# Optimization experiments

Measured on AMD Instinct MI355X. Metric: run time of the kernel, lower is better.

## Reference

```python
import jax, jax.numpy as jnp
import numpy as np

HID, NH, HD = 2048, 16, 128


def setup_inputs() -> dict:
    key = jax.random.key(0)
    ks = jax.random.split(key, 9)
    B, S = 2, 2048
    std = 0.02
    return {
        "hidden_states": jax.random.normal(ks[0], (B, S, HID), dtype=jnp.float32),
        "Wq": jax.random.normal(ks[1], (HID, HID), dtype=jnp.float32) * std,
        "bq": jnp.zeros((HID,), dtype=jnp.float32),
        "Wk": jax.random.normal(ks[2], (HID, HID), dtype=jnp.float32) * std,
        "bk": jnp.zeros((HID,), dtype=jnp.float32),
        "Wv": jax.random.normal(ks[3], (HID, HID), dtype=jnp.float32) * std,
        "bv": jnp.zeros((HID,), dtype=jnp.float32),
        "Wo": jax.random.normal(ks[4], (HID, HID), dtype=jnp.float32) * std,
        "bo": jnp.zeros((HID,), dtype=jnp.float32),
    }


def reference(hidden_states, Wq, bq, Wk, bk, Wv, bv, Wo, bo):
    B, S, _ = hidden_states.shape
    # torch Linear: x @ W.T + b
    def proj(W, b):
        y = hidden_states @ W.T + b
        return y.reshape(B, S, NH, HD).transpose(0, 2, 1, 3)  # (B, NH, S, HD)

    q = proj(Wq, bq)
    k = proj(Wk, bk)
    v = proj(Wv, bv)

    scale = jnp.float32(np.sqrt(HD))
    scores = jnp.einsum("bhqd,bhkd->bhqk", q, k) / scale  # (B, NH, S, S)
    causal = jnp.triu(jnp.ones((S, S), dtype=bool), k=1)
    scores = jnp.where(causal, jnp.float32(-jnp.inf), scores)
    weights = jax.nn.softmax(scores, axis=-1)
    out = jnp.einsum("bhqk,bhkd->bhqd", weights, v)  # (B, NH, S, HD)
    out = out.transpose(0, 2, 1, 3).reshape(B, S, HID)
    return out @ Wo.T + bo
```

## Files before the change

### kernel.cpp

```cpp
#include <hip/hip_runtime.h>
#include <hip/hip_bf16.h>

#define BATCH 2
#define SEQ   2048
#define HID_  2048
#define NH_   16
#define HD_   128

typedef __bf16 bf16x8 __attribute__((ext_vector_type(8)));
typedef float  f32x4  __attribute__((ext_vector_type(4)));

__device__ __forceinline__ unsigned short f32_to_bf16(float f) {
    unsigned int u = __builtin_bit_cast(unsigned int, f);
    unsigned int r = (u + 0x7fffu + ((u >> 16) & 1u)) >> 16;
    return (unsigned short)r;
}

__device__ __forceinline__ void gld_lds16(void* lds, const void* g) {
    __builtin_amdgcn_global_load_lds(
        (const __attribute__((address_space(1))) unsigned int*)g,
        (__attribute__((address_space(3))) unsigned int*)lds, 16, 0, 0);
}

__global__ void cvt_f32_bf16(const float* __restrict__ in,
                             unsigned short* __restrict__ out, int n4) {
    int i = blockIdx.x * blockDim.x + threadIdx.x;
    if (i >= n4) return;
    float4 a = reinterpret_cast<const float4*>(in)[i];
    ushort4 o;
    o.x = f32_to_bf16(a.x);
    o.y = f32_to_bf16(a.y);
    o.z = f32_to_bf16(a.z);
    o.w = f32_to_bf16(a.w);
    reinterpret_cast<ushort4*>(out)[i] = o;
}

enum { OUT_BF16 = 0, OUT_VT = 1, OUT_F32 = 2 };

template <int MODE>
__global__ __launch_bounds__(256)
void gemm_bt(const unsigned short* __restrict__ A,
             const unsigned short* __restrict__ B,
             const float* __restrict__ bias,
             void* __restrict__ Cout,
             int M, int N, int K) {
    const int tid  = threadIdx.x;
    const int lane = tid & 63;
    const int wid  = tid >> 6;
    const int wr   = wid >> 1;
    const int wc   = wid & 1;
    const int l16  = lane & 15;
    const int l4   = lane >> 4;

    const int row0 = blockIdx.y * 128;
    const int col0 = blockIdx.x * 128;

    __shared__ unsigned short As[128 * 32];
    __shared__ unsigned short Bs[128 * 32];

    f32x4 acc[4][4] = {};

    const int srow = tid >> 2;
    const int scol = (tid & 3) * 8;
    const unsigned short* Ag = A + (size_t)(row0 + srow) * K + scol;
    const unsigned short* Bg = B + (size_t)(col0 + srow) * K + scol;
    unsigned short* AsW = As + wid * 512;
    unsigned short* BsW = Bs + wid * 512;

    const unsigned short* AsR = As + (size_t)(wr * 64 + l16) * 32 + l4 * 8;
    const unsigned short* BsR = Bs + (size_t)(wc * 64 + l16) * 32 + l4 * 8;

    for (int k0 = 0; k0 < K; k0 += 32) {
        __syncthreads();
        gld_lds16(AsW,        Ag + k0);
        gld_lds16(AsW + 2048, Ag + (size_t)64 * K + k0);
        gld_lds16(BsW,        Bg + k0);
        gld_lds16(BsW + 2048, Bg + (size_t)64 * K + k0);
        __syncthreads();

        bf16x8 af[4], bfr[4];
#pragma unroll
        for (int i = 0; i < 4; ++i)
            af[i] = *reinterpret_cast<const bf16x8*>(AsR + i * 16 * 32);
#pragma unroll
        for (int j = 0; j < 4; ++j)
            bfr[j] = *reinterpret_cast<const bf16x8*>(BsR + j * 16 * 32);
#pragma unroll
        for (int i = 0; i < 4; ++i)
#pragma unroll
            for (int j = 0; j < 4; ++j)
                acc[i][j] = __builtin_amdgcn_mfma_f32_16x16x32_bf16(
                    af[i], bfr[j], acc[i][j], 0, 0, 0);
    }

    const int wrow0 = row0 + wr * 64;
    const int wcol0 = col0 + wc * 64;
#pragma unroll
    for (int j = 0; j < 4; ++j) {
        const int col = wcol0 + j * 16 + l16;
        const float bv = bias[col];
#pragma unroll
        for (int i = 0; i < 4; ++i) {
#pragma unroll
            for (int r = 0; r < 4; ++r) {
                const int row = wrow0 + i * 16 + l4 * 4 + r;
                const float v = acc[i][j][r] + bv;
                if (MODE == OUT_BF16) {
                    ((unsigned short*)Cout)[(size_t)row * N + col] = f32_to_bf16(v);
                } else if (MODE == OUT_F32) {
                    ((float*)Cout)[(size_t)row * N + col] = v;
                } else {
                    const int b = row >> 11, s = row & (SEQ - 1);
                    const int h = col >> 7,  d = col & (HD_ - 1);
                    ((unsigned short*)Cout)[((size_t)((b * NH_ + h) * HD_ + d)) * SEQ + s] =
                        f32_to_bf16(v);
                }
            }
        }
    }
}

__global__ __launch_bounds__(256, 2)
void attn_fwd(const unsigned short* __restrict__ Qm,
              const unsigned short* __restrict__ Km,
              const unsigned short* __restrict__ Vt,
              unsigned short* __restrict__ Om) {
    const int tid  = threadIdx.x;
    const int lane = tid & 63;
    const int wq   = tid >> 6;
    const int l16  = lane & 15;
    const int l4   = lane >> 4;

    const int bh = blockIdx.x;
    const int qt = (int)gridDim.y - 1 - (int)blockIdx.y;
    const int b  = bh >> 4;
    const int h  = bh & (NH_ - 1);

    const int qbase  = qt * 64 + wq * 16;
    const int ntiles = qt + 1;

    __shared__ unsigned short Ks[2][64 * 128];
    __shared__ unsigned short Vs[2][128 * 64];
    __shared__ unsigned short plds[4][16][68];

    const unsigned short* Kbh = Km + ((size_t)b * SEQ) * HID_ + h * HD_;
    const unsigned short* Vbh = Vt + (size_t)bh * HD_ * SEQ;

    auto stage = [&](int buf, int t) {
        const int kv0 = t * 64;
        {
            const int rl = lane >> 4;
            const int ck = lane & 15;
#pragma unroll
            for (int j = 0; j < 4; ++j) {
                const int r  = wq * 16 + 4 * j + rl;
                const int lc = ck ^ (r & 7);
                gld_lds16(&Ks[buf][(wq * 16 + 4 * j) * 128],
                          Kbh + (size_t)(kv0 + r) * HID_ + lc * 8);
            }
        }
        {
            const int rl = lane >> 3;
            const int ck = lane & 7;
#pragma unroll
            for (int j = 0; j < 4; ++j) {
                const int r  = wq * 32 + 8 * j + rl;
                const int lc = ck ^ (r & 7);
                gld_lds16(&Vs[buf][(wq * 32 + 8 * j) * 64],
                          Vbh + (size_t)r * SEQ + kv0 + lc * 8);
            }
        }
    };

    stage(0, 0);
    const unsigned short* Qbase =
        Qm + ((size_t)(b * SEQ + qbase + l16)) * HID_ + h * HD_ + l4 * 8;
    bf16x8 qf[4];
#pragma unroll
    for (int kb = 0; kb < 4; ++kb)
        qf[kb] = *reinterpret_cast<const bf16x8*>(Qbase + kb * 32);

    float mrow[4], lrow[4];
#pragma unroll
    for (int r = 0; r < 4; ++r) { mrow[r] = -__builtin_inff(); lrow[r] = 0.f; }
    f32x4 acc[8] = {};

    const float scale = 0.08838834764831845f;

    int buf = 0;
    for (int t = 0; t < ntiles; ++t) {
        __syncthreads();
        if (t + 1 < ntiles) stage(buf ^ 1, t + 1);

        const unsigned short* Kb0 = &Ks[buf][0];
        const unsigned short* Vb0 = &Vs[buf][0];
        const int kv0 = t * 64;
        const int sw  = l16 & 7;

        f32x4 sc[4];
#pragma unroll
        for (int ct = 0; ct < 4; ++ct) {
            f32x4 c = {};
#pragma unroll
            for (int kb = 0; kb < 4; ++kb) {
                bf16x8 kf = *reinterpret_cast<const bf16x8*>(
                    Kb0 + (ct * 16 + l16) * 128 + ((kb * 4 + l4) ^ sw) * 8);
                c = __builtin_amdgcn_mfma_f32_16x16x32_bf16(qf[kb], kf, c, 0, 0, 0);
            }
            sc[ct] = c;
        }

        if (t == ntiles - 1) {
#pragma unroll
            for (int ct = 0; ct < 4; ++ct) {
                const int col = kv0 + ct * 16 + l16;
#pragma unroll
                for (int r = 0; r < 4; ++r) {
                    float v = sc[ct][r] * scale;
                    const int qrow = qbase + l4 * 4 + r;
                    if (col > qrow) v = -__builtin_inff();
                    sc[ct][r] = v;
                }
            }
        } else {
#pragma unroll
            for (int ct = 0; ct < 4; ++ct)
#pragma unroll
                for (int r = 0; r < 4; ++r)
                    sc[ct][r] *= scale;
        }

        float tmax[4];
#pragma unroll
        for (int r = 0; r < 4; ++r) {
            float v = fmaxf(fmaxf(sc[0][r], sc[1][r]), fmaxf(sc[2][r], sc[3][r]));
#pragma unroll
            for (int off = 8; off >= 1; off >>= 1)
                v = fmaxf(v, __shfl_xor(v, off, 64));
            tmax[r] = v;
        }

        float alpha[4], rs[4];
#pragma unroll
        for (int r = 0; r < 4; ++r) {
            const float mn = fmaxf(mrow[r], tmax[r]);
            alpha[r] = __expf(mrow[r] - mn);
            mrow[r] = mn;
            rs[r] = 0.f;
        }

#pragma unroll
        for (int ct = 0; ct < 4; ++ct) {
#pragma unroll
            for (int r = 0; r < 4; ++r) {
                const float p = __expf(sc[ct][r] - mrow[r]);
                rs[r] += p;
                plds[wq][l4 * 4 + r][ct * 16 + l16] = f32_to_bf16(p);
            }
        }

#pragma unroll
        for (int r = 0; r < 4; ++r) {
#pragma unroll
            for (int off = 8; off >= 1; off >>= 1)
                rs[r] += __shfl_xor(rs[r], off, 64);
            lrow[r] = lrow[r] * alpha[r] + rs[r];
        }

#pragma unroll
        for (int dt = 0; dt < 8; ++dt)
#pragma unroll
            for (int r = 0; r < 4; ++r)
                acc[dt][r] *= alpha[r];

        asm volatile("s_waitcnt lgkmcnt(0)" ::: "memory");
        bf16x8 pf[2];
#pragma unroll
        for (int ks = 0; ks < 2; ++ks)
            pf[ks] = *reinterpret_cast<const bf16x8*>(&plds[wq][l16][ks * 32 + l4 * 8]);
#pragma unroll
        for (int dt = 0; dt < 8; ++dt) {
#pragma unroll
            for (int ks = 0; ks < 2; ++ks) {
                bf16x8 vf = *reinterpret_cast<const bf16x8*>(
                    Vb0 + (dt * 16 + l16) * 64 + ((ks * 4 + l4) ^ sw) * 8);
                acc[dt] = __builtin_amdgcn_mfma_f32_16x16x32_bf16(pf[ks], vf, acc[dt], 0, 0, 0);
            }
        }

        buf ^= 1;
    }

    unsigned short* Ob = Om + ((size_t)(b * SEQ + qbase)) * HID_ + h * HD_;
#pragma unroll
    for (int dt = 0; dt < 8; ++dt) {
#pragma unroll
        for (int r = 0; r < 4; ++r) {
            const int qrow = l4 * 4 + r;
            const float v = acc[dt][r] / lrow[r];
            Ob[(size_t)qrow * HID_ + dt * 16 + l16] = f32_to_bf16(v);
        }
    }
}

extern "C" void kernel_launch(void* const* d_in, const int* in_sizes, int n_in,
                              void* d_out, int out_size, void* d_ws, size_t ws_size,
                              hipStream_t stream) {
    const float* X  = (const float*)d_in[0];
    const float* Wq = (const float*)d_in[1];
    const float* bq = (const float*)d_in[2];
    const float* Wk = (const float*)d_in[3];
    const float* bk = (const float*)d_in[4];
    const float* Wv = (const float*)d_in[5];
    const float* bv = (const float*)d_in[6];
    const float* Wo = (const float*)d_in[7];
    const float* bo = (const float*)d_in[8];
    float* out = (float*)d_out;

    const size_t MK = (size_t)BATCH * SEQ * HID_;
    const size_t WK = (size_t)HID_ * HID_;

    unsigned short* ws  = (unsigned short*)d_ws;
    unsigned short* Xb  = ws;
    unsigned short* Wqb = Xb  + MK;
    unsigned short* Wkb = Wqb + WK;
    unsigned short* Wvb = Wkb + WK;
    unsigned short* Wob = Wvb + WK;
    unsigned short* Qb  = Wob + WK;
    unsigned short* Kb  = Qb  + MK;
    unsigned short* Vtb = Kb  + MK;
    unsigned short* AOb = Vtb + MK;

    auto cvt = [&](const float* src, unsigned short* dst, size_t n) {
        int n4 = (int)(n / 4);
        cvt_f32_bf16<<<(n4 + 255) / 256, 256, 0, stream>>>(src, dst, n4);
    };
    cvt(X,  Xb,  MK);
    cvt(Wq, Wqb, WK);
    cvt(Wk, Wkb, WK);
    cvt(Wv, Wvb, WK);
    cvt(Wo, Wob, WK);

    const int M = BATCH * SEQ;
    dim3 g(HID_ / 128, M / 128);

    gemm_bt<OUT_BF16><<<g, 256, 0, stream>>>(Xb, Wqb, bq, Qb,  M, HID_, HID_);
    gemm_bt<OUT_BF16><<<g, 256, 0, stream>>>(Xb, Wkb, bk, Kb,  M, HID_, HID_);
    gemm_bt<OUT_VT>  <<<g, 256, 0, stream>>>(Xb, Wvb, bv, Vtb, M, HID_, HID_);

    attn_fwd<<<dim3(BATCH * NH_, SEQ / 64), 256, 0, stream>>>(Qb, Kb, Vtb, AOb);

    gemm_bt<OUT_F32><<<g, 256, 0, stream>>>(AOb, Wob, bo, out, M, HID_, HID_);
}
```

Baseline: 455.4 us.

## Double-buffer GEMM loads, swizzle LDS, fuse QKV GEMMs, lazy softmax rescale

The GEMM main loop now double-buffers LDS tiles so the next K-slice loads while MFMAs run, and applies an XOR swizzle to LDS columns to cut bank conflicts. The Q, K and V projections become one launch over a 3x wider grid, with the output segment chosen per block. This relies on Wq, Wk and Wv sitting contiguously in the bf16 buffer. Flash attention skips rescaling the running max and accumulators unless the new tile max exceeds the old one by more than 8, trading exp/multiply work for a bounded risk of overflow in the accumulators.

Result: faster. 433.2 us (-4.9%).

```diff
diff --git a/kernel.cpp b/kernel.cpp
--- a/kernel.cpp
+++ b/kernel.cpp
@@ -35,64 +35,109 @@
     reinterpret_cast<ushort4*>(out)[i] = o;
 }
 
-enum { OUT_BF16 = 0, OUT_VT = 1, OUT_F32 = 2 };
-
-template <int MODE>
+#define GEMM_MAIN_LOOP                                                       \
+    const int K = HID_;                                                      \
+    const int tid  = threadIdx.x;                                            \
+    const int lane = tid & 63;                                               \
+    const int wid  = tid >> 6;                                               \
+    const int wr   = wid >> 1;                                               \
+    const int wc   = wid & 1;                                                \
+    const int l16  = lane & 15;                                              \
+    const int l4   = lane >> 4;                                              \
+    const int ckey = l16 & 3;                                                \
+    const int row0 = blockIdx.y * 128;                                       \
+    const int col0 = blockIdx.x * 128;                                       \
+    __shared__ unsigned short As[2][128 * 32];                               \
+    __shared__ unsigned short Bs[2][128 * 32];                               \
+    f32x4 acc[4][4] = {};                                                    \
+    const int srow = tid >> 2;                                               \
+    const int scol = ((tid & 3) ^ (srow & 3)) * 8;     \
+    const unsigned short* Ag = A + (size_t)(row0 + srow) * K + scol;         \
+    const unsigned short* Bg = B + (size_t)(col0 + srow) * K + scol;         \
+    auto stage = [&](int bb, int k0) {                                       \
+        gld_lds16(&As[bb][wid * 512],        Ag + k0);                       \
+        gld_lds16(&As[bb][2048 + wid * 512], Ag + (size_t)64 * K + k0);      \
+        gld_lds16(&Bs[bb][wid * 512],        Bg + k0);                       \
+        gld_lds16(&Bs[bb][2048 + wid * 512], Bg + (size_t)64 * K + k0);      \
+    };                                                                       \
+    stage(0, 0);                                                             \
+    int buf = 0;                                                             \
+    for (int k0 = 0; k0 < K; k0 += 32) {                                     \
+        const bool more = (k0 + 32) < K;                                     \
+        if (more) {                                                          \
+            stage(buf ^ 1, k0 + 32);                                         \
+            asm volatile("s_waitcnt vmcnt(4)" ::: "memory");                 \
+        } else {                                                             \
+            asm volatile("s_waitcnt vmcnt(0)" ::: "memory");                 \
+        }                                                                    \
+        __builtin_amdgcn_s_barrier();                                        \
+        const unsigned short* Ab = &As[buf][0];                              \
+        const unsigned short* Bb = &Bs[buf][0];                              \
+        bf16x8 af[4], bfr[4];                                                \
+        _Pragma("unroll")                                                    \
+        for (int i = 0; i < 4; ++i)                                          \
+            af[i] = *reinterpret_cast<const bf16x8*>(                        \
+                Ab + (wr * 64 + i * 16 + l16) * 32 + ((l4 ^ ckey) * 8));     \
+        _Pragma("unroll")                                                    \
+        for (int j = 0; j < 4; ++j)                                          \
+            bfr[j] = *reinterpret_cast<const bf16x8*>(                       \
+                Bb + (wc * 64 + j * 16 + l16) * 32 + ((l4 ^ ckey) * 8));     \
+        _Pragma("unroll")                                                    \
+        for (int i = 0; i < 4; ++i)                                          \
+            _Pragma("unroll")                                                \
+            for (int j = 0; j < 4; ++j)                                      \
+                acc[i][j] = __builtin_amdgcn_mfma_f32_16x16x32_bf16(         \
+                    af[i], bfr[j], acc[i][j], 0, 0, 0);                      \
+        asm volatile("s_waitcnt lgkmcnt(0)" ::: "memory");                   \
+        __builtin_amdgcn_s_barrier();                                        \
+        buf ^= 1;                                                            \
+    }
+
 __global__ __launch_bounds__(256)
-void gemm_bt(const unsigned short* __restrict__ A,
-             const unsigned short* __restrict__ B,
-             const float* __restrict__ bias,
-             void* __restrict__ Cout,
-             int M, int N, int K) {
-    const int tid  = threadIdx.x;
-    const int lane = tid & 63;
-    const int wid  = tid >> 6;
-    const int wr   = wid >> 1;
-    const int wc   = wid & 1;
-    const int l16  = lane & 15;
-    const int l4   = lane >> 4;
-
-    const int row0 = blockIdx.y * 128;
-    const int col0 = blockIdx.x * 128;
-
-    __shared__ unsigned short As[128 * 32];
-    __shared__ unsigned short Bs[128 * 32];
-
-    f32x4 acc[4][4] = {};
-
-    const int srow = tid >> 2;
-    const int scol = (tid & 3) * 8;
-    const unsigned short* Ag = A + (size_t)(row0 + srow) * K + scol;
-    const unsigned short* Bg = B + (size_t)(col0 + srow) * K + scol;
-    unsigned short* AsW = As + wid * 512;
-    unsigned short* BsW = Bs + wid * 512;
-
-    const unsigned short* AsR = As + (size_t)(wr * 64 + l16) * 32 + l4 * 8;
-    const unsigned short* BsR = Bs + (size_t)(wc * 64 + l16) * 32 + l4 * 8;
-
-    for (int k0 = 0; k0 < K; k0 += 32) {
-        __syncthreads();
-        gld_lds16(AsW,        Ag + k0);
-        gld_lds16(AsW + 2048, Ag + (size_t)64 * K + k0);
-        gld_lds16(BsW,        Bg + k0);
-        gld_lds16(BsW + 2048, Bg + (size_t)64 * K + k0);
-        __syncthreads();
-
-        bf16x8 af[4], bfr[4];
-#pragma unroll
-        for (int i = 0; i < 4; ++i)
-            af[i] = *reinterpret_cast<const bf16x8*>(AsR + i * 16 * 32);
-#pragma unroll
-        for (int j = 0; j < 4; ++j)
-            bfr[j] = *reinterpret_cast<const bf16x8*>(BsR + j * 16 * 32);
-#pragma unroll
-        for (int i = 0; i < 4; ++i)
-#pragma unroll
-            for (int j = 0; j < 4; ++j)
-                acc[i][j] = __builtin_amdgcn_mfma_f32_16x16x32_bf16(
-                    af[i], bfr[j], acc[i][j], 0, 0, 0);
-    }
-
+void gemm_qkv(const unsigned short* __restrict__ A,
+              const unsigned short* __restrict__ B,
+              const float* __restrict__ bq,
+              const float* __restrict__ bk,
+              const float* __restrict__ bv,
+              unsigned short* __restrict__ Qo,
+              unsigned short* __restrict__ Ko,
+              unsigned short* __restrict__ Vto) {
+    GEMM_MAIN_LOOP
+    const int seg = col0 >> 11;
+    const float* bias = (seg == 0) ? bq : (seg == 1) ? bk : bv;
+    const int wrow0 = row0 + wr * 64;
+    const int wcol0 = (col0 & (HID_ - 1)) + wc * 64;
+#pragma unroll
+    for (int j = 0; j < 4; ++j) {
+        const int col = wcol0 + j * 16 + l16;
+        const float bvv = bias[col];
+#pragma unroll
+        for (int i = 0; i < 4; ++i) {
+#pragma unroll
+            for (int r = 0; r < 4; ++r) {
+                const int row = wrow0 + i * 16 + l4 * 4 + r;
+                const float v = acc[i][j][r] + bvv;
+                if (seg == 0) {
+                    Qo[(size_t)row * HID_ + col] = f32_to_bf16(v);
+                } else if (seg == 1) {
+                    Ko[(size_t)row * HID_ + col] = f32_to_bf16(v);
+                } else {
+                    const int b = row >> 11, s = row & (SEQ - 1);
+                    const int h = col >> 7,  d = col & (HD_ - 1);
+                    Vto[((size_t)((b * NH_ + h) * HD_ + d)) * SEQ + s] =
+                        f32_to_bf16(v);
+                }
+            }
+        }
+    }
+}
+
+__global__ __launch_bounds__(256)
+void gemm_out(const unsigned short* __restrict__ A,
+              const unsigned short* __restrict__ B,
+              const float* __restrict__ bias,
+              float* __restrict__ Cout) {
+    GEMM_MAIN_LOOP
     const int wrow0 = row0 + wr * 64;
     const int wcol0 = col0 + wc * 64;
 #pragma unroll
@@ -104,17 +149,7 @@
 #pragma unroll
             for (int r = 0; r < 4; ++r) {
                 const int row = wrow0 + i * 16 + l4 * 4 + r;
-                const float v = acc[i][j][r] + bv;
-                if (MODE == OUT_BF16) {
-                    ((unsigned short*)Cout)[(size_t)row * N + col] = f32_to_bf16(v);
-                } else if (MODE == OUT_F32) {
-                    ((float*)Cout)[(size_t)row * N + col] = v;
-                } else {
-                    const int b = row >> 11, s = row & (SEQ - 1);
-                    const int h = col >> 7,  d = col & (HD_ - 1);
-                    ((unsigned short*)Cout)[((size_t)((b * NH_ + h) * HD_ + d)) * SEQ + s] =
-                        f32_to_bf16(v);
-                }
+                Cout[(size_t)row * HID_ + col] = acc[i][j][r] + bv;
             }
         }
     }
@@ -240,15 +275,25 @@
             tmax[r] = v;
         }
 
-        float alpha[4], rs[4];
-#pragma unroll
-        for (int r = 0; r < 4; ++r) {
-            const float mn = fmaxf(mrow[r], tmax[r]);
-            alpha[r] = __expf(mrow[r] - mn);
-            mrow[r] = mn;
-            rs[r] = 0.f;
-        }
-
+        bool need = false;
+#pragma unroll
+        for (int r = 0; r < 4; ++r) need = need || (tmax[r] > mrow[r] + 8.f);
+        if (__any(need)) {
+#pragma unroll
+            for (int r = 0; r < 4; ++r) {
+                const float mn = fmaxf(mrow[r], tmax[r]);
+                const float al = __expf(mrow[r] - mn);
+                mrow[r] = mn;
+                lrow[r] *= al;
+#pragma unroll
+                for (int dt = 0; dt < 8; ++dt)
+                    acc[dt][r] *= al;
+            }
+        }
+
+        float rs[4];
+#pragma unroll
+        for (int r = 0; r < 4; ++r) rs[r] = 0.f;
 #pragma unroll
         for (int ct = 0; ct < 4; ++ct) {
 #pragma unroll
@@ -264,14 +309,8 @@
 #pragma unroll
             for (int off = 8; off >= 1; off >>= 1)
                 rs[r] += __shfl_xor(rs[r], off, 64);
-            lrow[r] = lrow[r] * alpha[r] + rs[r];
-        }
-
-#pragma unroll
-        for (int dt = 0; dt < 8; ++dt)
-#pragma unroll
-            for (int r = 0; r < 4; ++r)
-                acc[dt][r] *= alpha[r];
+            lrow[r] += rs[r];
+        }
 
         asm volatile("s_waitcnt lgkmcnt(0)" ::: "memory");
         bf16x8 pf[2];
@@ -341,14 +380,11 @@
     cvt(Wv, Wvb, WK);
     cvt(Wo, Wob, WK);
 
-    const int M = BATCH * SEQ;
-    dim3 g(HID_ / 128, M / 128);
-
-    gemm_bt<OUT_BF16><<<g, 256, 0, stream>>>(Xb, Wqb, bq, Qb,  M, HID_, HID_);
-    gemm_bt<OUT_BF16><<<g, 256, 0, stream>>>(Xb, Wkb, bk, Kb,  M, HID_, HID_);
-    gemm_bt<OUT_VT>  <<<g, 256, 0, stream>>>(Xb, Wvb, bv, Vtb, M, HID_, HID_);
+    gemm_qkv<<<dim3(3 * HID_ / 128, BATCH * SEQ / 128), 256, 0, stream>>>(
+        Xb, Wqb, bq, bk, bv, Qb, Kb, Vtb);
 
     attn_fwd<<<dim3(BATCH * NH_, SEQ / 64), 256, 0, stream>>>(Qb, Kb, Vtb, AOb);
 
-    gemm_bt<OUT_F32><<<g, 256, 0, stream>>>(AOb, Wob, bo, out, M, HID_, HID_);
-}
+    gemm_out<<<dim3(HID_ / 128, BATCH * SEQ / 128), 256, 0, stream>>>(
+        AOb, Wob, bo, out);
+}
```
